# Performance work log

Hardware: AMD Instinct MI355X
Metric: run time of the kernel (lower is better)

The kernel has to match this reference:

```python
import jax, jax.numpy as jnp
import numpy as np

# Dims: N tokens, top_k K, E experts, d_model D, expert hidden H
N, K, E, D, H = 4096, 2, 8, 1024, 1024


def setup_inputs() -> dict:
    key = jax.random.key(0)
    k1, k2, k3, k4, k5, k6 = jax.random.split(key, 6)
    x = jax.random.normal(k1, (N, D), dtype=jnp.float32)
    expert_indices = jax.random.randint(k2, (N, K), 0, E, dtype=jnp.int32)
    ew = jax.random.uniform(k3, (N, K), dtype=jnp.float32)
    expert_weights = ew / ew.sum(-1, keepdims=True)  # router probs over top-k
    # histogram consistent with expert_indices (computed by the router in the real model)
    batch_size_per_expert = jnp.bincount(expert_indices.reshape(-1), length=E).astype(jnp.int32)
    w1 = jax.random.normal(k4, (E, D, H), dtype=jnp.float32) * (D ** -0.5)
    w3 = jax.random.normal(k5, (E, D, H), dtype=jnp.float32) * (D ** -0.5)
    w2 = jax.random.normal(k6, (E, H, D), dtype=jnp.float32) * (H ** -0.5)
    return {
        "x": x,
        "expert_weights": expert_weights,
        "expert_indices": expert_indices,
        "batch_size_per_expert": batch_size_per_expert,
        "w1": w1,
        "w2": w2,
        "w3": w3,
    }


def reference(x, expert_weights, expert_indices, batch_size_per_expert, w1, w2, w3):
    """Dropless MoE: sort token-copies by expert, grouped-GEMM SwiGLU, unpermute+combine."""
    nk = N * K
    flat_idx = expert_indices.reshape(nk)               # (N*K,)
    order = jnp.argsort(flat_idx)                        # stable sort -> permutation into expert order
    x_perm = x[order // K]                               # (N*K, D) gather source token per copy
    gs = batch_size_per_expert.astype(jnp.int32)         # grouped-GEMM group sizes, sums to N*K
    # per-expert SwiGLU MLP via grouped GEMM (rows of x_perm are contiguous per expert)
    h = jax.nn.silu(jax.lax.ragged_dot(x_perm, w1, gs)) * jax.lax.ragged_dot(x_perm, w3, gs)  # (N*K, H)
    out_perm = jax.lax.ragged_dot(h, w2, gs)             # (N*K, D)
    # unpermute: scatter rows back to original (token, k) order
    out_flat = jnp.zeros_like(x_perm).at[order].set(out_perm)  # (N*K, D)
    # weighted combine over top-k copies
    out = jnp.einsum("nk,nkd->nd", expert_weights, out_flat.reshape(N, K, D))
    return out
```

## Files before the change

### kernel.cpp

```cpp
#include <hip/hip_runtime.h>
#include <hip/hip_bf16.h>
#include <stdint.h>

#define N_TOK   4096
#define TOPK    2
#define N_EXP   8
#define D_MODEL 1024
#define H_DIM   1024
#define NK      (N_TOK * TOPK)
#define MAX_TILES 72

typedef __attribute__((ext_vector_type(8))) short bf16x8;
typedef __attribute__((ext_vector_type(4))) float f32x4;
typedef unsigned short bfbits;

__device__ inline bfbits f2bf_bits(float f) {
  union { float f; unsigned int u; } v; v.f = f;
  unsigned int r = v.u + 0x7FFFu + ((v.u >> 16) & 1u);
  return (bfbits)(r >> 16);
}
__device__ inline float bf2f(unsigned short u) {
  union { unsigned int u; float f; } v; v.u = ((unsigned int)u) << 16;
  return v.f;
}

__device__ inline void glds16(const bfbits* g, bfbits* l) {
  __builtin_amdgcn_global_load_lds(
      (const __attribute__((address_space(1))) void*)g,
      (__attribute__((address_space(3))) void*)l, 16, 0, 0);
}

__global__ void prepass_kernel(const float* __restrict__ x, const int* __restrict__ eidx,
                               const int* __restrict__ bspe,
                               const float* __restrict__ w1, const float* __restrict__ w2,
                               const float* __restrict__ w3,
                               bfbits* __restrict__ w1t, bfbits* __restrict__ w2t,
                               bfbits* __restrict__ w3t, bfbits* __restrict__ xb,
                               int* __restrict__ meta, int* __restrict__ row_src,
                               int* __restrict__ pos_of) {
  int z = blockIdx.z;
  int tid = threadIdx.x;
  if (z < 24) {
    const size_t MAT = (size_t)1024 * 1024;
    const float* src; bfbits* dst;
    if (z < 8)       { src = w1 + (size_t)z * MAT;        dst = w1t + (size_t)z * MAT; }
    else if (z < 16) { src = w3 + (size_t)(z - 8) * MAT;  dst = w3t + (size_t)(z - 8) * MAT; }
    else             { src = w2 + (size_t)(z - 16) * MAT; dst = w2t + (size_t)(z - 16) * MAT; }
    __shared__ bfbits tl[64][65];
    int r0 = blockIdx.y * 64, c0 = blockIdx.x * 64;
    for (int it = 0; it < 4; it++) {
      int r = (tid >> 4) + it * 16;
      int c = (tid & 15) * 4;
      float4 v = *(const float4*)&src[(size_t)(r0 + r) * 1024 + c0 + c];
      tl[r][c + 0] = f2bf_bits(v.x); tl[r][c + 1] = f2bf_bits(v.y);
      tl[r][c + 2] = f2bf_bits(v.z); tl[r][c + 3] = f2bf_bits(v.w);
    }
    __syncthreads();
    for (int it = 0; it < 4; it++) {
      int o = (tid >> 4) + it * 16;
      int r4 = (tid & 15) * 4;
      ushort4 v;
      v.x = tl[r4 + 0][o]; v.y = tl[r4 + 1][o];
      v.z = tl[r4 + 2][o]; v.w = tl[r4 + 3][o];
      *(ushort4*)&dst[(size_t)(c0 + o) * 1024 + r0 + r4] = v;
    }
  } else if (z < 40) {
    int i = ((z - 24) * 256 + blockIdx.y * 16 + blockIdx.x) * 256 + tid;
    float4 v = ((const float4*)x)[i];
    ushort4 o;
    o.x = f2bf_bits(v.x); o.y = f2bf_bits(v.y);
    o.z = f2bf_bits(v.z); o.w = f2bf_bits(v.w);
    ((ushort4*)xb)[i] = o;
  } else {
    if (blockIdx.x != 0 || blockIdx.y != 0) return;
    __shared__ int sm[162];
    __shared__ int scnt[N_EXP];
    if (tid == 0) {
      int acc = 0, nt = 0;
      for (int e = 0; e < N_EXP; e++) {
        sm[e] = acc;
        int g = bspe[e];
        for (int tt = 0; tt * 128 < g; tt++) {
          sm[18 + nt] = e;
          sm[90 + nt] = acc + tt * 128;
          nt++;
        }
        acc += g;
      }
      sm[8] = acc;
      sm[17] = nt;
      for (int i = nt; i < MAX_TILES; i++) { sm[18 + i] = 0; sm[90 + i] = 0; }
    }
    if (tid < N_EXP) scnt[tid] = 0;
    __syncthreads();
    for (int i = tid; i < NK; i += 256) {
      int e = eidx[i];
      int p = sm[e] + atomicAdd(&scnt[e], 1);
      row_src[p] = i;
      pos_of[i] = p;
    }
    if (tid < 162) meta[tid] = sm[tid];
  }
}

__global__ __launch_bounds__(256, 3) void gemm_swiglu_kernel(
    const bfbits* __restrict__ xb, const bfbits* __restrict__ w1t,
    const bfbits* __restrict__ w3t, const int* __restrict__ row_src,
    const int* __restrict__ meta, bfbits* __restrict__ hb) {
  int nt = meta[17];
  int bt = blockIdx.y;
  if (bt >= nt) return;
  int e = meta[18 + bt];
  int row0 = meta[90 + bt];
  int rows_end = meta[e + 1];
  int n0 = blockIdx.x * 64;

  __shared__ __align__(16) bfbits As[128 * 64];
  __shared__ __align__(16) bfbits B1s[64 * 64];
  __shared__ __align__(16) bfbits B3s[64 * 64];

  int tid = threadIdx.x, lane = tid & 63, wv = tid >> 6;
  int r8 = lane >> 3, jl = lane & 7;
  int jg = jl ^ r8;

  const bfbits* gp[8]; bfbits* lp[8];
  for (int j = 0; j < 8; j++) {
    int s = wv * 8 + j;
    if (s < 16) {
      int tok = row_src[row0 + s * 8 + r8] >> 1;
      gp[j] = xb + (size_t)tok * D_MODEL + jg * 8;
      lp[j] = As + s * 512;
    } else if (s < 24) {
      int b = s - 16;
      gp[j] = w1t + ((size_t)e * H_DIM + n0 + b * 8 + r8) * D_MODEL + jg * 8;
      lp[j] = B1s + b * 512;
    } else {
      int b = s - 24;
      gp[j] = w3t + ((size_t)e * H_DIM + n0 + b * 8 + r8) * D_MODEL + jg * 8;
      lp[j] = B3s + b * 512;
    }
  }

  const f32x4 fzero = {0.f, 0.f, 0.f, 0.f};
  f32x4 accg[4][2], accu[4][2];
  for (int i = 0; i < 4; i++)
    for (int j = 0; j < 2; j++) { accg[i][j] = fzero; accu[i][j] = fzero; }

  int mw = (wv & 1) * 64, nwv = (wv >> 1) * 32;
  int qd = lane >> 4, lr = lane & 15, lr7 = lr & 7;

  for (int kk = 0; kk < D_MODEL / 64; kk++) {
    int ko = kk * 64;
    for (int j = 0; j < 8; j++) glds16(gp[j] + ko, lp[j]);
    __syncthreads();
    for (int ks = 0; ks < 2; ks++) {
      int sb = ((ks * 4 + qd) ^ lr7) << 3;
      bf16x8 af[4], b1f[2], b3f[2];
      for (int mi = 0; mi < 4; mi++)
        af[mi] = *(const bf16x8*)&As[(mw + mi * 16 + lr) * 64 + sb];
      for (int ni = 0; ni < 2; ni++) {
        b1f[ni] = *(const bf16x8*)&B1s[(nwv + ni * 16 + lr) * 64 + sb];
        b3f[ni] = *(const bf16x8*)&B3s[(nwv + ni * 16 + lr) * 64 + sb];
      }
      for (int mi = 0; mi < 4; mi++)
        for (int ni = 0; ni < 2; ni++) {
          accg[mi][ni] = __builtin_amdgcn_mfma_f32_16x16x32_bf16(af[mi], b1f[ni], accg[mi][ni], 0, 0, 0);
          accu[mi][ni] = __builtin_amdgcn_mfma_f32_16x16x32_bf16(af[mi], b3f[ni], accu[mi][ni], 0, 0, 0);
        }
    }
    __syncthreads();
  }

  for (int mi = 0; mi < 4; mi++) {
    int rbase = row0 + mw + mi * 16 + qd * 4;
    for (int r = 0; r < 4; r++) {
      int grow = rbase + r;
      if (grow < rows_end) {
        for (int ni = 0; ni < 2; ni++) {
          float gg = accg[mi][ni][r], u = accu[mi][ni][r];
          float h = gg / (1.f + __expf(-gg)) * u;
          hb[(size_t)grow * H_DIM + n0 + nwv + ni * 16 + lr] = f2bf_bits(h);
        }
      }
    }
  }
}

__global__ __launch_bounds__(256, 4) void gemm_out_kernel(
    const bfbits* __restrict__ hb, const bfbits* __restrict__ w2t,
    const int* __restrict__ meta, bfbits* __restrict__ out_perm) {
  int nt = meta[17];
  int bt = blockIdx.y;
  if (bt >= nt) return;
  int e = meta[18 + bt];
  int row0 = meta[90 + bt];
  int rows_end = meta[e + 1];
  int n0 = blockIdx.x * 64;

  __shared__ __align__(16) bfbits As[128 * 64];
  __shared__ __align__(16) bfbits Bs[64 * 64];

  int tid = threadIdx.x, lane = tid & 63, wv = tid >> 6;
  int r8 = lane >> 3, jl = lane & 7;
  int jg = jl ^ r8;

  const bfbits* gp[6]; bfbits* lp[6];
  for (int j = 0; j < 6; j++) {
    int s = wv * 6 + j;
    if (s < 16) {
      gp[j] = hb + (size_t)(row0 + s * 8 + r8) * H_DIM + jg * 8;
      lp[j] = As + s * 512;
    } else {
      int b = s - 16;
      gp[j] = w2t + ((size_t)e * D_MODEL + n0 + b * 8 + r8) * H_DIM + jg * 8;
      lp[j] = Bs + b * 512;
    }
  }

  const f32x4 fzero = {0.f, 0.f, 0.f, 0.f};
  f32x4 acc[4][2];
  for (int i = 0; i < 4; i++)
    for (int j = 0; j < 2; j++) acc[i][j] = fzero;

  int mw = (wv & 1) * 64, nwv = (wv >> 1) * 32;
  int qd = lane >> 4, lr = lane & 15, lr7 = lr & 7;

  for (int kk = 0; kk < H_DIM / 64; kk++) {
    int ko = kk * 64;
    for (int j = 0; j < 6; j++) glds16(gp[j] + ko, lp[j]);
    __syncthreads();
    for (int ks = 0; ks < 2; ks++) {
      int sb = ((ks * 4 + qd) ^ lr7) << 3;
      bf16x8 af[4], bfr[2];
      for (int mi = 0; mi < 4; mi++)
        af[mi] = *(const bf16x8*)&As[(mw + mi * 16 + lr) * 64 + sb];
      for (int ni = 0; ni < 2; ni++)
        bfr[ni] = *(const bf16x8*)&Bs[(nwv + ni * 16 + lr) * 64 + sb];
      for (int mi = 0; mi < 4; mi++)
        for (int ni = 0; ni < 2; ni++)
          acc[mi][ni] = __builtin_amdgcn_mfma_f32_16x16x32_bf16(af[mi], bfr[ni], acc[mi][ni], 0, 0, 0);
    }
    __syncthreads();
  }

  for (int mi = 0; mi < 4; mi++) {
    int rbase = row0 + mw + mi * 16 + qd * 4;
    for (int r = 0; r < 4; r++) {
      int grow = rbase + r;
      if (grow < rows_end) {
        for (int ni = 0; ni < 2; ni++)
          out_perm[(size_t)grow * D_MODEL + n0 + nwv + ni * 16 + lr] = f2bf_bits(acc[mi][ni][r]);
      }
    }
  }
}

__global__ void combine_kernel(const ushort4* __restrict__ out_perm,
                               const int* __restrict__ pos_of,
                               const float* __restrict__ ew, float4* __restrict__ out) {
  int i = blockIdx.x * 256 + threadIdx.x;
  int tok = i >> 8;
  int col = i & 255;
  int p0 = pos_of[2 * tok], p1 = pos_of[2 * tok + 1];
  float w0 = ew[2 * tok], w1 = ew[2 * tok + 1];
  ushort4 a = out_perm[(size_t)p0 * 256 + col];
  ushort4 b = out_perm[(size_t)p1 * 256 + col];
  float4 o;
  o.x = w0 * bf2f(a.x) + w1 * bf2f(b.x);
  o.y = w0 * bf2f(a.y) + w1 * bf2f(b.y);
  o.z = w0 * bf2f(a.z) + w1 * bf2f(b.z);
  o.w = w0 * bf2f(a.w) + w1 * bf2f(b.w);
  out[i] = o;
}

extern "C" void kernel_launch(void* const* d_in, const int* in_sizes, int n_in,
                              void* d_out, int out_size, void* d_ws, size_t ws_size,
                              hipStream_t stream) {
  const float* x  = (const float*)d_in[0];
  const float* ew = (const float*)d_in[1];
  const int* eidx = (const int*)d_in[2];
  const int* bspe = (const int*)d_in[3];
  const float* w1 = (const float*)d_in[4];
  const float* w2 = (const float*)d_in[5];
  const float* w3 = (const float*)d_in[6];
  float* out = (float*)d_out;

  char* ws = (char*)d_ws;
  const size_t MB = 1024 * 1024;
  bfbits* w1t   = (bfbits*)(ws);
  bfbits* w3t   = (bfbits*)(ws + 16 * MB);
  bfbits* w2t   = (bfbits*)(ws + 32 * MB);
  bfbits* xb    = (bfbits*)(ws + 48 * MB);
  bfbits* hb    = (bfbits*)(ws + 56 * MB);
  bfbits* out_perm = (bfbits*)(ws);
  int* row_src  = (int*)(ws + 72 * MB);
  int* pos_of   = (int*)(ws + 72 * MB + 32 * 1024);
  int* meta     = (int*)(ws + 72 * MB + 64 * 1024);

  prepass_kernel<<<dim3(16, 16, 41), 256, 0, stream>>>(
      x, eidx, bspe, w1, w2, w3, w1t, w2t, w3t, xb, meta, row_src, pos_of);
  gemm_swiglu_kernel<<<dim3(H_DIM / 64, MAX_TILES), 256, 0, stream>>>(
      xb, w1t, w3t, row_src, meta, hb);
  gemm_out_kernel<<<dim3(D_MODEL / 64, MAX_TILES), 256, 0, stream>>>(
      hb, w2t, meta, out_perm);
  combine_kernel<<<(N_TOK * D_MODEL / 4) / 256, 256, 0, stream>>>(
      (const ushort4*)out_perm, pos_of, ew, (float4*)out);
}
```

Baseline: 248.6 us.

## Overlap w2 transpose-convert with SwiGLU GEMM and aggregate routing atomics

Moves the fp32-to-bf16 transpose of w2 out of the prepass and into extra blocks of the SwiGLU GEMM launch, so that conversion can overlap with GEMM work instead of serialising ahead of it. The x conversion blocks now each process 16 chunks, and the routing block uses wave ballots so that one atomic per expert per wave replaces one atomic per element. Weight tile loads are batched before the LDS stores. The risks are contention between the transpose blocks and the GEMM tiles for bandwidth and LDS, and a longer tail in the GEMM launch.

New measurement: 269.7 us. +8.5%, slower.

```diff
diff --git a/kernel.cpp b/kernel.cpp
--- a/kernel.cpp
+++ b/kernel.cpp
@@ -30,55 +30,50 @@
       (__attribute__((address_space(3))) void*)l, 16, 0, 0);
 }
 
+__device__ inline void trans_tile64(const float* __restrict__ src, bfbits* __restrict__ dst,
+                                    int r0, int c0, bfbits (*tl)[65], int tid) {
+  float4 v[4];
+  for (int it = 0; it < 4; it++) {
+    int r = (tid >> 4) + it * 16;
+    int c = (tid & 15) * 4;
+    v[it] = *(const float4*)&src[(size_t)(r0 + r) * 1024 + c0 + c];
+  }
+  for (int it = 0; it < 4; it++) {
+    int r = (tid >> 4) + it * 16;
+    int c = (tid & 15) * 4;
+    tl[r][c + 0] = f2bf_bits(v[it].x); tl[r][c + 1] = f2bf_bits(v[it].y);
+    tl[r][c + 2] = f2bf_bits(v[it].z); tl[r][c + 3] = f2bf_bits(v[it].w);
+  }
+  __syncthreads();
+  for (int it = 0; it < 4; it++) {
+    int o = (tid >> 4) + it * 16;
+    int r4 = (tid & 15) * 4;
+    ushort4 w;
+    w.x = tl[r4 + 0][o]; w.y = tl[r4 + 1][o];
+    w.z = tl[r4 + 2][o]; w.w = tl[r4 + 3][o];
+    *(ushort4*)&dst[(size_t)(c0 + o) * 1024 + r0 + r4] = w;
+  }
+}
+
 __global__ void prepass_kernel(const float* __restrict__ x, const int* __restrict__ eidx,
                                const int* __restrict__ bspe,
-                               const float* __restrict__ w1, const float* __restrict__ w2,
-                               const float* __restrict__ w3,
-                               bfbits* __restrict__ w1t, bfbits* __restrict__ w2t,
-                               bfbits* __restrict__ w3t, bfbits* __restrict__ xb,
+                               const float* __restrict__ w1, const float* __restrict__ w3,
+                               bfbits* __restrict__ w1t, bfbits* __restrict__ w3t,
+                               bfbits* __restrict__ xb,
                                int* __restrict__ meta, int* __restrict__ row_src,
                                int* __restrict__ pos_of) {
   int z = blockIdx.z;
   int tid = threadIdx.x;
-  if (z < 24) {
-    const size_t MAT = (size_t)1024 * 1024;
-    const float* src; bfbits* dst;
-    if (z < 8)       { src = w1 + (size_t)z * MAT;        dst = w1t + (size_t)z * MAT; }
-    else if (z < 16) { src = w3 + (size_t)(z - 8) * MAT;  dst = w3t + (size_t)(z - 8) * MAT; }
-    else             { src = w2 + (size_t)(z - 16) * MAT; dst = w2t + (size_t)(z - 16) * MAT; }
-    __shared__ bfbits tl[64][65];
-    int r0 = blockIdx.y * 64, c0 = blockIdx.x * 64;
-    for (int it = 0; it < 4; it++) {
-      int r = (tid >> 4) + it * 16;
-      int c = (tid & 15) * 4;
-      float4 v = *(const float4*)&src[(size_t)(r0 + r) * 1024 + c0 + c];
-      tl[r][c + 0] = f2bf_bits(v.x); tl[r][c + 1] = f2bf_bits(v.y);
-      tl[r][c + 2] = f2bf_bits(v.z); tl[r][c + 3] = f2bf_bits(v.w);
-    }
-    __syncthreads();
-    for (int it = 0; it < 4; it++) {
-      int o = (tid >> 4) + it * 16;
-      int r4 = (tid & 15) * 4;
-      ushort4 v;
-      v.x = tl[r4 + 0][o]; v.y = tl[r4 + 1][o];
-      v.z = tl[r4 + 2][o]; v.w = tl[r4 + 3][o];
-      *(ushort4*)&dst[(size_t)(c0 + o) * 1024 + r0 + r4] = v;
-    }
-  } else if (z < 40) {
-    int i = ((z - 24) * 256 + blockIdx.y * 16 + blockIdx.x) * 256 + tid;
-    float4 v = ((const float4*)x)[i];
-    ushort4 o;
-    o.x = f2bf_bits(v.x); o.y = f2bf_bits(v.y);
-    o.z = f2bf_bits(v.z); o.w = f2bf_bits(v.w);
-    ((ushort4*)xb)[i] = o;
-  } else {
+  if (z == 0) {
     if (blockIdx.x != 0 || blockIdx.y != 0) return;
     __shared__ int sm[162];
     __shared__ int scnt[N_EXP];
+    int lane = tid & 63;
     if (tid == 0) {
       int acc = 0, nt = 0;
       for (int e = 0; e < N_EXP; e++) {
         sm[e] = acc;
+        sm[9 + e] = 0;
         int g = bspe[e];
         for (int tt = 0; tt * 128 < g; tt++) {
           sm[18 + nt] = e;
@@ -93,33 +88,74 @@
     }
     if (tid < N_EXP) scnt[tid] = 0;
     __syncthreads();
-    for (int i = tid; i < NK; i += 256) {
+    unsigned long long below = (1ULL << lane) - 1ULL;
+    for (int it = 0; it < NK / 256; it++) {
+      int i = it * 256 + tid;
       int e = eidx[i];
-      int p = sm[e] + atomicAdd(&scnt[e], 1);
+      int p = 0;
+      for (int ee = 0; ee < N_EXP; ee++) {
+        bool mine = (e == ee);
+        unsigned long long m = __ballot(mine);
+        if (m != 0ULL) {
+          int first = __ffsll(m) - 1;
+          int base = 0;
+          if (lane == first) base = atomicAdd(&scnt[ee], __popcll(m));
+          base = __shfl(base, first);
+          if (mine) p = sm[ee] + base + __popcll(m & below);
+        }
+      }
       row_src[p] = i;
       pos_of[i] = p;
     }
+    __syncthreads();
     if (tid < 162) meta[tid] = sm[tid];
+  } else if (z < 17) {
+    int zm = z - 1;
+    const size_t MAT = (size_t)1024 * 1024;
+    const float* src = (zm < 8) ? (w1 + (size_t)zm * MAT) : (w3 + (size_t)(zm - 8) * MAT);
+    bfbits* dst = (zm < 8) ? (w1t + (size_t)zm * MAT) : (w3t + (size_t)(zm - 8) * MAT);
+    __shared__ bfbits tl[64][65];
+    trans_tile64(src, dst, blockIdx.y * 64, blockIdx.x * 64, tl, tid);
+  } else {
+    int b = blockIdx.y * 16 + blockIdx.x;
+    for (int it = 0; it < 16; it++) {
+      int i = b * 4096 + it * 256 + tid;
+      float4 v = ((const float4*)x)[i];
+      ushort4 o;
+      o.x = f2bf_bits(v.x); o.y = f2bf_bits(v.y);
+      o.z = f2bf_bits(v.z); o.w = f2bf_bits(v.w);
+      ((ushort4*)xb)[i] = o;
+    }
   }
 }
 
 __global__ __launch_bounds__(256, 3) void gemm_swiglu_kernel(
     const bfbits* __restrict__ xb, const bfbits* __restrict__ w1t,
     const bfbits* __restrict__ w3t, const int* __restrict__ row_src,
-    const int* __restrict__ meta, bfbits* __restrict__ hb) {
+    const int* __restrict__ meta, bfbits* __restrict__ hb,
+    const float* __restrict__ w2, bfbits* __restrict__ w2t) {
+  __shared__ __align__(16) bfbits As[128 * 64];
+  __shared__ __align__(16) bfbits B1s[64 * 64];
+  __shared__ __align__(16) bfbits B3s[64 * 64];
+  int tid = threadIdx.x;
+  int bt = blockIdx.y;
+  if (bt >= MAX_TILES) {
+    int tid2 = (bt - MAX_TILES) * 16 + blockIdx.x;
+    const size_t MAT = (size_t)1024 * 1024;
+    int mat = tid2 >> 8, rem = tid2 & 255;
+    bfbits (*tl)[65] = (bfbits (*)[65])As;
+    trans_tile64(w2 + (size_t)mat * MAT, w2t + (size_t)mat * MAT,
+                 (rem >> 4) * 64, (rem & 15) * 64, tl, tid);
+    return;
+  }
   int nt = meta[17];
-  int bt = blockIdx.y;
   if (bt >= nt) return;
   int e = meta[18 + bt];
   int row0 = meta[90 + bt];
   int rows_end = meta[e + 1];
   int n0 = blockIdx.x * 64;
 
-  __shared__ __align__(16) bfbits As[128 * 64];
-  __shared__ __align__(16) bfbits B1s[64 * 64];
-  __shared__ __align__(16) bfbits B3s[64 * 64];
-
-  int tid = threadIdx.x, lane = tid & 63, wv = tid >> 6;
+  int lane = tid & 63, wv = tid >> 6;
   int r8 = lane >> 3, jl = lane & 7;
   int jg = jl ^ r8;
 
@@ -297,10 +333,10 @@
   int* pos_of   = (int*)(ws + 72 * MB + 32 * 1024);
   int* meta     = (int*)(ws + 72 * MB + 64 * 1024);
 
-  prepass_kernel<<<dim3(16, 16, 41), 256, 0, stream>>>(
-      x, eidx, bspe, w1, w2, w3, w1t, w2t, w3t, xb, meta, row_src, pos_of);
-  gemm_swiglu_kernel<<<dim3(H_DIM / 64, MAX_TILES), 256, 0, stream>>>(
-      xb, w1t, w3t, row_src, meta, hb);
+  prepass_kernel<<<dim3(16, 16, 18), 256, 0, stream>>>(
+      x, eidx, bspe, w1, w3, w1t, w3t, xb, meta, row_src, pos_of);
+  gemm_swiglu_kernel<<<dim3(H_DIM / 64, MAX_TILES + 128), 256, 0, stream>>>(
+      xb, w1t, w3t, row_src, meta, hb, w2, w2t);
   gemm_out_kernel<<<dim3(D_MODEL / 64, MAX_TILES), 256, 0, stream>>>(
       hb, w2t, meta, out_perm);
   combine_kernel<<<(N_TOK * D_MODEL / 4) / 256, 256, 0, stream>>>(
```
